# Optimization experiments

Hardware: AMD Instinct MI355X
Metric: run time of the kernel (lower is better)

## Reference

```python
import jax, jax.numpy as jnp
from jax import lax
import numpy as np

H, W = 240, 304
IN_CH, OUT_CH, K = 16, 32, 3
B = 8
N_PER = 65536
N = B * N_PER
CIN = IN_CH + 2  # pos + neg + features


def setup_inputs() -> dict:
    key = jax.random.key(0)
    k1, k2, k3, k4, k5 = jax.random.split(key, 5)
    # events columns: x, y, t in [0,1); polarity in {0,1}
    xyt = jax.random.uniform(k1, (N, 3), dtype=jnp.float32)
    pol = jax.random.randint(k2, (N, 1), 0, 2).astype(jnp.float32)
    events = jnp.concatenate([xyt, pol], axis=1)
    features = jax.random.normal(k3, (N, IN_CH), dtype=jnp.float32)
    offsets = (jnp.arange(1, B + 1, dtype=jnp.int64) * N_PER)  # cumulative counts
    # SubmanifoldConvolution params: one [CIN, OUT_CH] matrix per filter offset -> HWIO
    fan_in = K * K * CIN
    weight = jax.random.normal(k4, (K, K, CIN, OUT_CH), dtype=jnp.float32) / np.sqrt(fan_in)
    bias = jax.random.normal(k5, (OUT_CH,), dtype=jnp.float32) * 0.01
    return {"events": events, "features": features, "weight": weight,
            "bias": bias, "offsets": offsets}


def reference(events, features, weight, bias, offsets):
    n = events.shape[0]
    b = offsets.shape[0]
    # offset2batch: row i belongs to first sample whose cumulative offset exceeds i
    batch = jnp.searchsorted(offsets, jnp.arange(n, dtype=offsets.dtype), side="right").astype(jnp.int32)
    pos = events[:, 3:4]
    neg = 1.0 - pos
    sparse = jnp.concatenate([pos, neg, features], axis=1)  # [N, CIN]
    # yx = events[:, [1, 0]] scaled by (h, w), rounded to grid coords
    yi = jnp.clip(jnp.round(events[:, 1] * H).astype(jnp.int32), 0, H - 1)
    xi = jnp.clip(jnp.round(events[:, 0] * W).astype(jnp.int32), 0, W - 1)
    key = (batch * H + yi) * W + xi  # linear site id, [N]
    nseg = b * H * W
    # scn InputLayer mode=4: average features of duplicate coordinates
    feat_sum = jax.ops.segment_sum(sparse, key, num_segments=nseg)  # [nseg, CIN]
    cnt = jax.ops.segment_sum(jnp.ones((n,), sparse.dtype), key, num_segments=nseg)
    dense = feat_sum / jnp.maximum(cnt, 1.0)[:, None]
    dense = dense.reshape(b, H, W, CIN)  # zeros at inactive sites
    # Submanifold 3x3 conv: inactive neighbors are zero, so a dense SAME conv
    # evaluated only at active sites matches the submanifold rulebook math.
    out = lax.conv_general_dilated(dense, weight, window_strides=(1, 1),
                                   padding="SAME",
                                   dimension_numbers=("NHWC", "HWIO", "NHWC"))
    out = out.reshape(nseg, OUT_CH)
    # OutputLayer: read back per input row (active sites only), add bias there
    f = out[key] + bias  # [N, OUT_CH]
    return f
```

## Files before the change

### kernel.cpp

```cpp
#include <hip/hip_runtime.h>

#define Hh 240
#define Ww 304
#define IN_CH 16
#define OUT_CH 32
#define Bb 8
#define N_PER 65536
#define N_EV (Bb * N_PER)
#define CIN (IN_CH + 2)
#define NSEG (Bb * Hh * Ww)
#define NBLK 570

#define TW 32
#define TH 8
#define HW_ 34
#define HH_ 10
#define NXT_TILES 10
#define NYT_TILES 30
#define OPITCH 33

typedef __attribute__((ext_vector_type(8))) short bf16x8;
typedef __attribute__((ext_vector_type(4))) float f32x4;

__device__ __forceinline__ unsigned short f2bf(float x) {
  unsigned u = __float_as_uint(x);
  unsigned r = u + 0x7fffu + ((u >> 16) & 1u);
  return (unsigned short)(r >> 16);
}
__device__ __forceinline__ float bf2f(unsigned short b) {
  return __uint_as_float(((unsigned)b) << 16);
}

__global__ __launch_bounds__(256) void hist_rank_kernel(
    const float* __restrict__ events, const int* __restrict__ offsets,
    int* __restrict__ hist, int* __restrict__ keyArr, int* __restrict__ rankArr) {
  int i = blockIdx.x * blockDim.x + threadIdx.x;
  float4 ev = ((const float4*)events)[i];
  int yi = (int)rintf(ev.y * (float)Hh);
  yi = min(max(yi, 0), Hh - 1);
  int xi = (int)rintf(ev.x * (float)Ww);
  xi = min(max(xi, 0), Ww - 1);
  int b = 0;
#pragma unroll
  for (int j = 0; j < Bb; j++) b += (offsets[j] <= i) ? 1 : 0;
  int key = (b * Hh + yi) * Ww + xi;
  int pol = (ev.w != 0.0f) ? 1 : 0;
  keyArr[i] = key | (pol << 31);
  rankArr[i] = atomicAdd(&hist[key], 1);
}

__global__ __launch_bounds__(256) void scan1_kernel(
    const int* __restrict__ hist, int* __restrict__ baseLocal,
    int* __restrict__ blockSum) {
  __shared__ int lds[256];
  int b = blockIdx.x, t = threadIdx.x;
  int idx = b * 1024 + t * 4;
  int4 v = *(const int4*)(hist + idx);
  int s0 = v.x, s1 = s0 + v.y, s2 = s1 + v.z, s3 = s2 + v.w;
  lds[t] = s3;
  __syncthreads();
  int val = s3;
  for (int off = 1; off < 256; off <<= 1) {
    int n = (t >= off) ? lds[t - off] : 0;
    __syncthreads();
    val += n;
    lds[t] = val;
    __syncthreads();
  }
  int excl = val - s3;
  int4 o;
  o.x = excl; o.y = excl + s0; o.z = excl + s1; o.w = excl + s2;
  *(int4*)(baseLocal + idx) = o;
  if (t == 255) blockSum[b] = val;
}

__global__ __launch_bounds__(1024) void scan2_kernel(
    const int* __restrict__ blockSum, int* __restrict__ blockOffset) {
  __shared__ int lds[1024];
  int t = threadIdx.x;
  int v = (t < NBLK) ? blockSum[t] : 0;
  lds[t] = v;
  __syncthreads();
  int val = v;
  for (int off = 1; off < 1024; off <<= 1) {
    int n = (t >= off) ? lds[t - off] : 0;
    __syncthreads();
    val += n;
    lds[t] = val;
    __syncthreads();
  }
  if (t < NBLK) blockOffset[t] = val - v;
  if (t == 0) blockOffset[NBLK] = lds[1023];
}

__global__ __launch_bounds__(256) void prep_weights_kernel(
    const float* __restrict__ weight, unsigned short* __restrict__ wprep) {
  int tid = threadIdx.x;
#pragma unroll
  for (int it = 0; it < 24; it++) {
    int idx = it * 256 + tid;
    int ky = idx >> 11;
    int rem = idx & 2047;
    int n = rem >> 6;
    int kl = rem & 63;
    unsigned short v = 0;
    if (kl < 54) {
      int kx = kl / 18, ci = kl - kx * 18;
      v = f2bf(weight[((ky * 3 + kx) * CIN + ci) * OUT_CH + n]);
    }
    wprep[idx] = v;
  }
}

__global__ __launch_bounds__(256) void scatter_idx_kernel(
    const int* __restrict__ keyArr, const int* __restrict__ rankArr,
    const int* __restrict__ baseLocal, const int* __restrict__ blockOffset,
    int* __restrict__ sortedMeta) {
  int i = blockIdx.x * blockDim.x + threadIdx.x;
  int meta = keyArr[i];
  int key = meta & 0x7fffffff;
  int pos = baseLocal[key] + blockOffset[key >> 10] + rankArr[i];
  sortedMeta[pos] = i | (meta & 0x80000000);
}

__global__ __launch_bounds__(256) void fused_conv_kernel(
    const float* __restrict__ features, const int* __restrict__ sortedMeta,
    const int* __restrict__ baseLocal, const int* __restrict__ blockOffset,
    const unsigned short* __restrict__ wprep, const float* __restrict__ bias,
    float* __restrict__ out) {
  __shared__ unsigned smem[128 * OPITCH];
  __shared__ int ibase[TH * TW];
  __shared__ int icnt[TH * TW];

  int blk = blockIdx.x;
  int xt = blk % NXT_TILES;
  int rem = blk / NXT_TILES;
  int yt = rem % NYT_TILES;
  int b = rem / NYT_TILES;
  int x0 = xt * TW, y0 = yt * TH;
  int tid = threadIdx.x;

  if (tid < 12) smem[3060 + tid] = 0;

  for (int h = tid; h < HH_ * HW_; h += 256) {
    int hy = h / HW_, hx = h % HW_;
    int gy = y0 - 1 + hy, gx = x0 - 1 + hx;
    float acc[CIN];
#pragma unroll
    for (int k = 0; k < CIN; k++) acc[k] = 0.0f;
    int c = 0, base = 0;
    if (gy >= 0 && gy < Hh && gx >= 0 && gx < Ww) {
      int p = (b * Hh + gy) * Ww + gx;
      int bo = blockOffset[p >> 10];
      base = baseLocal[p] + bo;
      int nxt = ((p & 1023) != 1023) ? (baseLocal[p + 1] + bo)
                                     : blockOffset[(p >> 10) + 1];
      c = nxt - base;
      for (int j = 0; j < c; j++) {
        int e = sortedMeta[base + j];
        float pol = (float)((unsigned)e >> 31);
        acc[0] += pol;
        acc[1] += 1.0f - pol;
        const float4* f =
            (const float4*)(features + (size_t)(e & 0x7fffffff) * IN_CH);
        float4 f0 = f[0], f1 = f[1], f2 = f[2], f3 = f[3];
        acc[2] += f0.x;  acc[3] += f0.y;  acc[4] += f0.z;  acc[5] += f0.w;
        acc[6] += f1.x;  acc[7] += f1.y;  acc[8] += f1.z;  acc[9] += f1.w;
        acc[10] += f2.x; acc[11] += f2.y; acc[12] += f2.z; acc[13] += f2.w;
        acc[14] += f3.x; acc[15] += f3.y; acc[16] += f3.z; acc[17] += f3.w;
      }
    }
    float inv = 1.0f / fmaxf((float)c, 1.0f);
    unsigned* row = smem + 9 * h;
#pragma unroll
    for (int k = 0; k < 9; k++)
      row[k] = (unsigned)f2bf(acc[2 * k] * inv) |
               ((unsigned)f2bf(acc[2 * k + 1] * inv) << 16);
    if (hx >= 1 && hx <= TW && hy >= 1 && hy <= TH) {
      int t = (hy - 1) * TW + (hx - 1);
      ibase[t] = base;
      icnt[t] = c;
    }
  }
  __syncthreads();

  int wv = tid >> 6, lane = tid & 63;
  int quad = lane >> 4, lrow = lane & 15;

  f32x4 accf[4][2];
#pragma unroll
  for (int i = 0; i < 4; i++)
#pragma unroll
    for (int nt = 0; nt < 2; nt++) accf[i][nt] = (f32x4){0.f, 0.f, 0.f, 0.f};

  const unsigned* hp = smem;
#pragma unroll
  for (int ky = 0; ky < 3; ky++) {
    bf16x8 bfr[2][2];
#pragma unroll
    for (int kh = 0; kh < 2; kh++)
#pragma unroll
      for (int nt = 0; nt < 2; nt++) {
        int n = nt * 16 + lrow;
        bfr[kh][nt] = *(const bf16x8*)(wprep + ((ky * 32 + n) << 6) +
                                       kh * 32 + quad * 8);
      }
#pragma unroll
    for (int i = 0; i < 4; i++) {
      int t0 = (wv * 4 + i) * 16;
      int ox = (t0 & 31) + lrow;
      int oy = t0 >> 5;
      int idx0 = ((oy + ky) * HW_ + ox) * CIN;
#pragma unroll
      for (int kh = 0; kh < 2; kh++) {
        union { bf16x8 v; unsigned u[4]; } a;
        int ui = (idx0 >> 1) + kh * 16 + quad * 4;
        a.u[0] = hp[ui]; a.u[1] = hp[ui + 1];
        a.u[2] = hp[ui + 2]; a.u[3] = hp[ui + 3];
        accf[i][0] = __builtin_amdgcn_mfma_f32_16x16x32_bf16(
            a.v, bfr[kh][0], accf[i][0], 0, 0, 0);
        accf[i][1] = __builtin_amdgcn_mfma_f32_16x16x32_bf16(
            a.v, bfr[kh][1], accf[i][1], 0, 0, 0);
      }
    }
  }
  __syncthreads();

  float* outsh = (float*)smem;
  float bn0 = bias[lrow], bn1 = bias[16 + lrow];
  int gx = x0 + (tid & 31);
  int c = icnt[tid];
  int base = ibase[tid];
#pragma unroll
  for (int ch = 0; ch < 2; ch++) {
#pragma unroll
    for (int ii = 0; ii < 2; ii++) {
      int i = ch * 2 + ii;
      int lidx = ii * 16 + quad * 4;
      int row = wv * 32 + lidx;
#pragma unroll
      for (int r = 0; r < 4; r++) {
        outsh[(row + r) * OPITCH + lrow] = accf[i][0][r] + bn0;
        outsh[(row + r) * OPITCH + 16 + lrow] = accf[i][1][r] + bn1;
      }
    }
    __syncthreads();
    if (((tid >> 5) & 1) == ch && gx < Ww && c > 0) {
      int row = (tid >> 6) * 32 + ((tid & 63) - ch * 32);
      const float* rp = outsh + row * OPITCH;
      float4 o0 = make_float4(rp[0], rp[1], rp[2], rp[3]);
      float4 o1 = make_float4(rp[4], rp[5], rp[6], rp[7]);
      float4 o2 = make_float4(rp[8], rp[9], rp[10], rp[11]);
      float4 o3 = make_float4(rp[12], rp[13], rp[14], rp[15]);
      float4 o4 = make_float4(rp[16], rp[17], rp[18], rp[19]);
      float4 o5 = make_float4(rp[20], rp[21], rp[22], rp[23]);
      float4 o6 = make_float4(rp[24], rp[25], rp[26], rp[27]);
      float4 o7 = make_float4(rp[28], rp[29], rp[30], rp[31]);
      for (int j = 0; j < c; j++) {
        int ev = sortedMeta[base + j] & 0x7fffffff;
        float4* op = (float4*)(out + (size_t)ev * OUT_CH);
        op[0] = o0; op[1] = o1; op[2] = o2; op[3] = o3;
        op[4] = o4; op[5] = o5; op[6] = o6; op[7] = o7;
      }
    }
    __syncthreads();
  }
}

extern "C" void kernel_launch(void* const* d_in, const int* in_sizes, int n_in,
                              void* d_out, int out_size, void* d_ws,
                              size_t ws_size, hipStream_t stream) {
  const float* events = (const float*)d_in[0];
  const float* features = (const float*)d_in[1];
  const float* weight = (const float*)d_in[2];
  const float* bias = (const float*)d_in[3];
  const int* offsets = (const int*)d_in[4];
  float* out = (float*)d_out;

  int* sortedMeta = (int*)d_ws;
  int* keyArr = sortedMeta + N_EV;
  int* rankArr = keyArr + N_EV;
  int* hist = rankArr + N_EV;
  int* baseLocal = hist + NSEG;
  int* blockOffset = baseLocal + NSEG;
  int* blockSum = blockOffset + 1024;
  unsigned short* wprep = (unsigned short*)(blockSum + 1024);

  hipMemsetAsync(hist, 0, (size_t)NSEG * sizeof(int), stream);

  hist_rank_kernel<<<N_EV / 256, 256, 0, stream>>>(events, offsets, hist,
                                                   keyArr, rankArr);
  prep_weights_kernel<<<1, 256, 0, stream>>>(weight, wprep);
  scan1_kernel<<<NBLK, 256, 0, stream>>>(hist, baseLocal, blockSum);
  scan2_kernel<<<1, 1024, 0, stream>>>(blockSum, blockOffset);
  scatter_idx_kernel<<<N_EV / 256, 256, 0, stream>>>(
      keyArr, rankArr, baseLocal, blockOffset, sortedMeta);
  fused_conv_kernel<<<Bb * NYT_TILES * NXT_TILES, 256, 0, stream>>>(
      features, sortedMeta, baseLocal, blockOffset, wprep, bias, out);
}
```

Baseline: 193.2 us.

## Distribute halo event gathering across threads with LDS atomics; fuse weight prep into scan2

The conv kernel's halo gather no longer gives each thread one pixel to loop over serially. It now builds per-row prefix sums of event counts and hands out individual events to threads. Each thread binary-searches for its event's pixel and accumulates features into a shared-memory fp32 buffer with LDS atomics. This evens out load across threads and makes feature reads more coalesced, at the cost of atomic contention, extra syncs and more LDS use, which may lower occupancy. Weight preparation is also merged into the scan2 launch as a second block, removing one kernel launch.

```diff
diff --git a/kernel.cpp b/kernel.cpp
--- a/kernel.cpp
+++ b/kernel.cpp
@@ -15,6 +15,7 @@
 #define TH 8
 #define HW_ 34
 #define HH_ 10
+#define HALO_PIX (HH_ * HW_)
 #define NXT_TILES 10
 #define NYT_TILES 30
 #define OPITCH 33
@@ -26,9 +27,6 @@
   unsigned u = __float_as_uint(x);
   unsigned r = u + 0x7fffu + ((u >> 16) & 1u);
   return (unsigned short)(r >> 16);
-}
-__device__ __forceinline__ float bf2f(unsigned short b) {
-  return __uint_as_float(((unsigned)b) << 16);
 }
 
 __global__ __launch_bounds__(256) void hist_rank_kernel(
@@ -74,10 +72,28 @@
   if (t == 255) blockSum[b] = val;
 }
 
-__global__ __launch_bounds__(1024) void scan2_kernel(
-    const int* __restrict__ blockSum, int* __restrict__ blockOffset) {
+__global__ __launch_bounds__(1024) void scan2_weights_kernel(
+    const int* __restrict__ blockSum, int* __restrict__ blockOffset,
+    const float* __restrict__ weight, unsigned short* __restrict__ wprep) {
+  int t = threadIdx.x;
+  if (blockIdx.x == 1) {
+#pragma unroll
+    for (int it = 0; it < 6; it++) {
+      int idx = it * 1024 + t;
+      int ky = idx >> 11;
+      int rem = idx & 2047;
+      int n = rem >> 6;
+      int kl = rem & 63;
+      unsigned short v = 0;
+      if (kl < 54) {
+        int kx = kl / 18, ci = kl - kx * 18;
+        v = f2bf(weight[((ky * 3 + kx) * CIN + ci) * OUT_CH + n]);
+      }
+      wprep[idx] = v;
+    }
+    return;
+  }
   __shared__ int lds[1024];
-  int t = threadIdx.x;
   int v = (t < NBLK) ? blockSum[t] : 0;
   lds[t] = v;
   __syncthreads();
@@ -91,25 +107,6 @@
   }
   if (t < NBLK) blockOffset[t] = val - v;
   if (t == 0) blockOffset[NBLK] = lds[1023];
-}
-
-__global__ __launch_bounds__(256) void prep_weights_kernel(
-    const float* __restrict__ weight, unsigned short* __restrict__ wprep) {
-  int tid = threadIdx.x;
-#pragma unroll
-  for (int it = 0; it < 24; it++) {
-    int idx = it * 256 + tid;
-    int ky = idx >> 11;
-    int rem = idx & 2047;
-    int n = rem >> 6;
-    int kl = rem & 63;
-    unsigned short v = 0;
-    if (kl < 54) {
-      int kx = kl / 18, ci = kl - kx * 18;
-      v = f2bf(weight[((ky * 3 + kx) * CIN + ci) * OUT_CH + n]);
-    }
-    wprep[idx] = v;
-  }
 }
 
 __global__ __launch_bounds__(256) void scatter_idx_kernel(
@@ -128,9 +125,12 @@
     const int* __restrict__ baseLocal, const int* __restrict__ blockOffset,
     const unsigned short* __restrict__ wprep, const float* __restrict__ bias,
     float* __restrict__ out) {
-  __shared__ unsigned smem[128 * OPITCH];
-  __shared__ int ibase[TH * TW];
-  __shared__ int icnt[TH * TW];
+  __shared__ float haloAcc[HALO_PIX * CIN];
+  __shared__ unsigned haloBf[3072];
+  __shared__ int pixBase[HALO_PIX];
+  __shared__ int pixCnt[HALO_PIX];
+  __shared__ int rowStart[HH_];
+  __shared__ int rowPfx[HH_ + 1];
 
   int blk = blockIdx.x;
   int xt = blk % NXT_TILES;
@@ -140,47 +140,79 @@
   int x0 = xt * TW, y0 = yt * TH;
   int tid = threadIdx.x;
 
-  if (tid < 12) smem[3060 + tid] = 0;
-
-  for (int h = tid; h < HH_ * HW_; h += 256) {
+  if (tid < 12) haloBf[3060 + tid] = 0;
+
+  for (int h = tid; h < HALO_PIX; h += 256) {
     int hy = h / HW_, hx = h % HW_;
     int gy = y0 - 1 + hy, gx = x0 - 1 + hx;
-    float acc[CIN];
-#pragma unroll
-    for (int k = 0; k < CIN; k++) acc[k] = 0.0f;
-    int c = 0, base = 0;
-    if (gy >= 0 && gy < Hh && gx >= 0 && gx < Ww) {
+    int base = 0, c = 0;
+    bool valid = (gy >= 0 && gy < Hh && gx >= 0 && gx < Ww);
+    if (valid) {
       int p = (b * Hh + gy) * Ww + gx;
       int bo = blockOffset[p >> 10];
       base = baseLocal[p] + bo;
       int nxt = ((p & 1023) != 1023) ? (baseLocal[p + 1] + bo)
                                      : blockOffset[(p >> 10) + 1];
       c = nxt - base;
-      for (int j = 0; j < c; j++) {
-        int e = sortedMeta[base + j];
-        float pol = (float)((unsigned)e >> 31);
-        acc[0] += pol;
-        acc[1] += 1.0f - pol;
-        const float4* f =
-            (const float4*)(features + (size_t)(e & 0x7fffffff) * IN_CH);
-        float4 f0 = f[0], f1 = f[1], f2 = f[2], f3 = f[3];
-        acc[2] += f0.x;  acc[3] += f0.y;  acc[4] += f0.z;  acc[5] += f0.w;
-        acc[6] += f1.x;  acc[7] += f1.y;  acc[8] += f1.z;  acc[9] += f1.w;
-        acc[10] += f2.x; acc[11] += f2.y; acc[12] += f2.z; acc[13] += f2.w;
-        acc[14] += f3.x; acc[15] += f3.y; acc[16] += f3.z; acc[17] += f3.w;
-      }
-    }
-    float inv = 1.0f / fmaxf((float)c, 1.0f);
-    unsigned* row = smem + 9 * h;
+    }
+    pixBase[h] = valid ? base : (gx < 0 ? 0 : 0x7fffffff);
+    pixCnt[h] = c;
+#pragma unroll
+    for (int k = 0; k < CIN; k++) haloAcc[h * CIN + k] = 0.0f;
+  }
+  __syncthreads();
+
+  if (tid < HH_) {
+    int s = 0;
+#pragma unroll
+    for (int x = 0; x < HW_; x++) s += pixCnt[tid * HW_ + x];
+    rowPfx[tid + 1] = s;
+    rowStart[tid] = pixBase[tid * HW_ + ((x0 == 0) ? 1 : 0)];
+  }
+  if (tid == 0) rowPfx[0] = 0;
+  __syncthreads();
+  if (tid == 0) {
+#pragma unroll
+    for (int r = 1; r <= HH_; r++) rowPfx[r] += rowPfx[r - 1];
+  }
+  __syncthreads();
+  int T = rowPfx[HH_];
+
+  for (int t = tid; t < T; t += 256) {
+    int r = 0;
+    while (r < HH_ - 1 && rowPfx[r + 1] <= t) ++r;
+    int q = rowStart[r] + (t - rowPfx[r]);
+    int lo = r * HW_, hi = lo + HW_ - 1;
+    while (lo < hi) {
+      int mid = (lo + hi + 1) >> 1;
+      if (pixBase[mid] <= q) lo = mid; else hi = mid - 1;
+    }
+    int meta = sortedMeta[q];
+    float pol = (float)((unsigned)meta >> 31);
+    int e = meta & 0x7fffffff;
+    const float4* f = (const float4*)(features + (size_t)e * IN_CH);
+    float4 f0 = f[0], f1 = f[1], f2 = f[2], f3 = f[3];
+    float* hA = haloAcc + lo * CIN;
+    atomicAdd(hA + 0, pol);
+    atomicAdd(hA + 1, 1.0f - pol);
+    atomicAdd(hA + 2, f0.x);  atomicAdd(hA + 3, f0.y);
+    atomicAdd(hA + 4, f0.z);  atomicAdd(hA + 5, f0.w);
+    atomicAdd(hA + 6, f1.x);  atomicAdd(hA + 7, f1.y);
+    atomicAdd(hA + 8, f1.z);  atomicAdd(hA + 9, f1.w);
+    atomicAdd(hA + 10, f2.x); atomicAdd(hA + 11, f2.y);
+    atomicAdd(hA + 12, f2.z); atomicAdd(hA + 13, f2.w);
+    atomicAdd(hA + 14, f3.x); atomicAdd(hA + 15, f3.y);
+    atomicAdd(hA + 16, f3.z); atomicAdd(hA + 17, f3.w);
+  }
+  __syncthreads();
+
+  for (int h = tid; h < HALO_PIX; h += 256) {
+    float inv = 1.0f / fmaxf((float)pixCnt[h], 1.0f);
+    unsigned* row = haloBf + 9 * h;
 #pragma unroll
     for (int k = 0; k < 9; k++)
-      row[k] = (unsigned)f2bf(acc[2 * k] * inv) |
-               ((unsigned)f2bf(acc[2 * k + 1] * inv) << 16);
-    if (hx >= 1 && hx <= TW && hy >= 1 && hy <= TH) {
-      int t = (hy - 1) * TW + (hx - 1);
-      ibase[t] = base;
-      icnt[t] = c;
-    }
+      row[k] = (unsigned)f2bf(haloAcc[h * CIN + 2 * k] * inv) |
+               ((unsigned)f2bf(haloAcc[h * CIN + 2 * k + 1] * inv) << 16);
   }
   __syncthreads();
 
@@ -193,7 +225,7 @@
 #pragma unroll
     for (int nt = 0; nt < 2; nt++) accf[i][nt] = (f32x4){0.f, 0.f, 0.f, 0.f};
 
-  const unsigned* hp = smem;
+  const unsigned* hp = haloBf;
 #pragma unroll
   for (int ky = 0; ky < 3; ky++) {
     bf16x8 bfr[2][2];
@@ -226,11 +258,12 @@
   }
   __syncthreads();
 
-  float* outsh = (float*)smem;
+  float* outsh = haloAcc;
   float bn0 = bias[lrow], bn1 = bias[16 + lrow];
   int gx = x0 + (tid & 31);
-  int c = icnt[tid];
-  int base = ibase[tid];
+  int hint = ((tid >> 5) + 1) * HW_ + (tid & 31) + 1;
+  int c = pixCnt[hint];
+  int base = pixBase[hint];
 #pragma unroll
   for (int ch = 0; ch < 2; ch++) {
 #pragma unroll
@@ -290,9 +323,9 @@
 
   hist_rank_kernel<<<N_EV / 256, 256, 0, stream>>>(events, offsets, hist,
                                                    keyArr, rankArr);
-  prep_weights_kernel<<<1, 256, 0, stream>>>(weight, wprep);
   scan1_kernel<<<NBLK, 256, 0, stream>>>(hist, baseLocal, blockSum);
-  scan2_kernel<<<1, 1024, 0, stream>>>(blockSum, blockOffset);
+  scan2_weights_kernel<<<2, 1024, 0, stream>>>(blockSum, blockOffset, weight,
+                                               wprep);
   scatter_idx_kernel<<<N_EV / 256, 256, 0, stream>>>(
       keyArr, rankArr, baseLocal, blockOffset, sortedMeta);
   fused_conv_kernel<<<Bb * NYT_TILES * NXT_TILES, 256, 0, stream>>>(
```

New measurement: 239.5 us. 1.24x slower.

## Scatter bf16 feature records in sorted order and fuse weight prep into scan

Applied to the files above, without the earlier changes.

The scatter kernel now writes each event's polarity/index metadata and bf16-packed features into a record array ordered by grid site, so the conv's halo accumulation reads contiguous records instead of gathering fp32 features by random index. Key and rank are stored together as an int2, weight preparation runs as a second block of the scan2 launch, and the halo loop issues both pixel lookups before accumulating. This trades random gathers in the conv for heavier random writes in scatter and rounds features to bf16 before averaging, which adds precision error.

```diff
diff --git a/kernel.cpp b/kernel.cpp
--- a/kernel.cpp
+++ b/kernel.cpp
@@ -15,6 +15,7 @@
 #define TH 8
 #define HW_ 34
 #define HH_ 10
+#define HALO_PIX (HH_ * HW_)
 #define NXT_TILES 10
 #define NYT_TILES 30
 #define OPITCH 33
@@ -30,10 +31,13 @@
 __device__ __forceinline__ float bf2f(unsigned short b) {
   return __uint_as_float(((unsigned)b) << 16);
 }
+__device__ __forceinline__ unsigned pk2(float a, float b) {
+  return (unsigned)f2bf(a) | ((unsigned)f2bf(b) << 16);
+}
 
 __global__ __launch_bounds__(256) void hist_rank_kernel(
     const float* __restrict__ events, const int* __restrict__ offsets,
-    int* __restrict__ hist, int* __restrict__ keyArr, int* __restrict__ rankArr) {
+    int* __restrict__ hist, int2* __restrict__ kr) {
   int i = blockIdx.x * blockDim.x + threadIdx.x;
   float4 ev = ((const float4*)events)[i];
   int yi = (int)rintf(ev.y * (float)Hh);
@@ -45,8 +49,8 @@
   for (int j = 0; j < Bb; j++) b += (offsets[j] <= i) ? 1 : 0;
   int key = (b * Hh + yi) * Ww + xi;
   int pol = (ev.w != 0.0f) ? 1 : 0;
-  keyArr[i] = key | (pol << 31);
-  rankArr[i] = atomicAdd(&hist[key], 1);
+  int rank = atomicAdd(&hist[key], 1);
+  kr[i] = make_int2(key | (pol << 31), rank);
 }
 
 __global__ __launch_bounds__(256) void scan1_kernel(
@@ -74,10 +78,28 @@
   if (t == 255) blockSum[b] = val;
 }
 
-__global__ __launch_bounds__(1024) void scan2_kernel(
-    const int* __restrict__ blockSum, int* __restrict__ blockOffset) {
+__global__ __launch_bounds__(1024) void scan2_weights_kernel(
+    const int* __restrict__ blockSum, int* __restrict__ blockOffset,
+    const float* __restrict__ weight, unsigned short* __restrict__ wprep) {
+  int t = threadIdx.x;
+  if (blockIdx.x == 1) {
+#pragma unroll
+    for (int it = 0; it < 6; it++) {
+      int idx = it * 1024 + t;
+      int ky = idx >> 11;
+      int rem = idx & 2047;
+      int n = rem >> 6;
+      int kl = rem & 63;
+      unsigned short v = 0;
+      if (kl < 54) {
+        int kx = kl / 18, ci = kl - kx * 18;
+        v = f2bf(weight[((ky * 3 + kx) * CIN + ci) * OUT_CH + n]);
+      }
+      wprep[idx] = v;
+    }
+    return;
+  }
   __shared__ int lds[1024];
-  int t = threadIdx.x;
   int v = (t < NBLK) ? blockSum[t] : 0;
   lds[t] = v;
   __syncthreads();
@@ -93,38 +115,55 @@
   if (t == 0) blockOffset[NBLK] = lds[1023];
 }
 
-__global__ __launch_bounds__(256) void prep_weights_kernel(
-    const float* __restrict__ weight, unsigned short* __restrict__ wprep) {
-  int tid = threadIdx.x;
-#pragma unroll
-  for (int it = 0; it < 24; it++) {
-    int idx = it * 256 + tid;
-    int ky = idx >> 11;
-    int rem = idx & 2047;
-    int n = rem >> 6;
-    int kl = rem & 63;
-    unsigned short v = 0;
-    if (kl < 54) {
-      int kx = kl / 18, ci = kl - kx * 18;
-      v = f2bf(weight[((ky * 3 + kx) * CIN + ci) * OUT_CH + n]);
-    }
-    wprep[idx] = v;
-  }
-}
-
-__global__ __launch_bounds__(256) void scatter_idx_kernel(
-    const int* __restrict__ keyArr, const int* __restrict__ rankArr,
+__global__ __launch_bounds__(256) void scatter_rec_kernel(
+    const float* __restrict__ features, const int2* __restrict__ kr,
     const int* __restrict__ baseLocal, const int* __restrict__ blockOffset,
-    int* __restrict__ sortedMeta) {
+    uint4* __restrict__ sortedRec, int* __restrict__ sortedMeta) {
   int i = blockIdx.x * blockDim.x + threadIdx.x;
-  int meta = keyArr[i];
-  int key = meta & 0x7fffffff;
-  int pos = baseLocal[key] + blockOffset[key >> 10] + rankArr[i];
-  sortedMeta[pos] = i | (meta & 0x80000000);
+  int2 m = kr[i];
+  int key = m.x & 0x7fffffff;
+  int pos = baseLocal[key] + blockOffset[key >> 10] + m.y;
+  const float4* f = (const float4*)(features + (size_t)i * IN_CH);
+  float4 f0 = f[0], f1 = f[1], f2 = f[2], f3 = f[3];
+  unsigned meta = (unsigned)i | ((unsigned)m.x & 0x80000000u);
+  uint4* R = sortedRec + (size_t)pos * 3;
+  R[0] = make_uint4(meta, pk2(f0.x, f0.y), pk2(f0.z, f0.w), pk2(f1.x, f1.y));
+  R[1] = make_uint4(pk2(f1.z, f1.w), pk2(f2.x, f2.y), pk2(f2.z, f2.w),
+                    pk2(f3.x, f3.y));
+  R[2] = make_uint4(pk2(f3.z, f3.w), 0, 0, 0);
+  sortedMeta[pos] = (int)meta;
+}
+
+__device__ __forceinline__ void accum_pixel(unsigned* smem,
+                                            const uint4* __restrict__ sortedRec,
+                                            int h, int base, int c) {
+  float acc[CIN];
+#pragma unroll
+  for (int k = 0; k < CIN; k++) acc[k] = 0.0f;
+  for (int j = 0; j < c; j++) {
+    const uint4* R = sortedRec + (size_t)(base + j) * 3;
+    uint4 r0 = R[0], r1 = R[1];
+    unsigned d8 = ((const unsigned*)R)[8];
+    float pol = (float)(r0.x >> 31);
+    acc[0] += pol;
+    acc[1] += 1.0f - pol;
+    acc[2]  += bf2f((unsigned short)r0.y);  acc[3]  += bf2f((unsigned short)(r0.y >> 16));
+    acc[4]  += bf2f((unsigned short)r0.z);  acc[5]  += bf2f((unsigned short)(r0.z >> 16));
+    acc[6]  += bf2f((unsigned short)r0.w);  acc[7]  += bf2f((unsigned short)(r0.w >> 16));
+    acc[8]  += bf2f((unsigned short)r1.x);  acc[9]  += bf2f((unsigned short)(r1.x >> 16));
+    acc[10] += bf2f((unsigned short)r1.y);  acc[11] += bf2f((unsigned short)(r1.y >> 16));
+    acc[12] += bf2f((unsigned short)r1.z);  acc[13] += bf2f((unsigned short)(r1.z >> 16));
+    acc[14] += bf2f((unsigned short)r1.w);  acc[15] += bf2f((unsigned short)(r1.w >> 16));
+    acc[16] += bf2f((unsigned short)d8);    acc[17] += bf2f((unsigned short)(d8 >> 16));
+  }
+  float inv = 1.0f / fmaxf((float)c, 1.0f);
+  unsigned* row = smem + 9 * h;
+#pragma unroll
+  for (int k = 0; k < 9; k++) row[k] = pk2(acc[2 * k] * inv, acc[2 * k + 1] * inv);
 }
 
 __global__ __launch_bounds__(256) void fused_conv_kernel(
-    const float* __restrict__ features, const int* __restrict__ sortedMeta,
+    const uint4* __restrict__ sortedRec, const int* __restrict__ sortedMeta,
     const int* __restrict__ baseLocal, const int* __restrict__ blockOffset,
     const unsigned short* __restrict__ wprep, const float* __restrict__ bias,
     float* __restrict__ out) {
@@ -142,44 +181,49 @@
 
   if (tid < 12) smem[3060 + tid] = 0;
 
-  for (int h = tid; h < HH_ * HW_; h += 256) {
-    int hy = h / HW_, hx = h % HW_;
+  int hA = tid, hB = tid + 256;
+  bool hasB = hB < HALO_PIX;
+  int baseA = 0, cA = 0, baseB = 0, cB = 0;
+  {
+    int hy = hA / HW_, hx = hA % HW_;
     int gy = y0 - 1 + hy, gx = x0 - 1 + hx;
-    float acc[CIN];
-#pragma unroll
-    for (int k = 0; k < CIN; k++) acc[k] = 0.0f;
-    int c = 0, base = 0;
     if (gy >= 0 && gy < Hh && gx >= 0 && gx < Ww) {
       int p = (b * Hh + gy) * Ww + gx;
       int bo = blockOffset[p >> 10];
-      base = baseLocal[p] + bo;
+      baseA = baseLocal[p] + bo;
       int nxt = ((p & 1023) != 1023) ? (baseLocal[p + 1] + bo)
                                      : blockOffset[(p >> 10) + 1];
-      c = nxt - base;
-      for (int j = 0; j < c; j++) {
-        int e = sortedMeta[base + j];
-        float pol = (float)((unsigned)e >> 31);
-        acc[0] += pol;
-        acc[1] += 1.0f - pol;
-        const float4* f =
-            (const float4*)(features + (size_t)(e & 0x7fffffff) * IN_CH);
-        float4 f0 = f[0], f1 = f[1], f2 = f[2], f3 = f[3];
-        acc[2] += f0.x;  acc[3] += f0.y;  acc[4] += f0.z;  acc[5] += f0.w;
-        acc[6] += f1.x;  acc[7] += f1.y;  acc[8] += f1.z;  acc[9] += f1.w;
-        acc[10] += f2.x; acc[11] += f2.y; acc[12] += f2.z; acc[13] += f2.w;
-        acc[14] += f3.x; acc[15] += f3.y; acc[16] += f3.z; acc[17] += f3.w;
-      }
-    }
-    float inv = 1.0f / fmaxf((float)c, 1.0f);
-    unsigned* row = smem + 9 * h;
-#pragma unroll
-    for (int k = 0; k < 9; k++)
-      row[k] = (unsigned)f2bf(acc[2 * k] * inv) |
-               ((unsigned)f2bf(acc[2 * k + 1] * inv) << 16);
+      cA = nxt - baseA;
+    }
+  }
+  if (hasB) {
+    int hy = hB / HW_, hx = hB % HW_;
+    int gy = y0 - 1 + hy, gx = x0 - 1 + hx;
+    if (gy >= 0 && gy < Hh && gx >= 0 && gx < Ww) {
+      int p = (b * Hh + gy) * Ww + gx;
+      int bo = blockOffset[p >> 10];
+      baseB = baseLocal[p] + bo;
+      int nxt = ((p & 1023) != 1023) ? (baseLocal[p + 1] + bo)
+                                     : blockOffset[(p >> 10) + 1];
+      cB = nxt - baseB;
+    }
+  }
+  accum_pixel(smem, sortedRec, hA, baseA, cA);
+  if (hasB) accum_pixel(smem, sortedRec, hB, baseB, cB);
+  {
+    int hy = hA / HW_, hx = hA % HW_;
     if (hx >= 1 && hx <= TW && hy >= 1 && hy <= TH) {
       int t = (hy - 1) * TW + (hx - 1);
-      ibase[t] = base;
-      icnt[t] = c;
+      ibase[t] = baseA;
+      icnt[t] = cA;
+    }
+  }
+  if (hasB) {
+    int hy = hB / HW_, hx = hB % HW_;
+    if (hx >= 1 && hx <= TW && hy >= 1 && hy <= TH) {
+      int t = (hy - 1) * TW + (hx - 1);
+      ibase[t] = baseB;
+      icnt[t] = cB;
     }
   }
   __syncthreads();
@@ -277,10 +321,10 @@
   const int* offsets = (const int*)d_in[4];
   float* out = (float*)d_out;
 
-  int* sortedMeta = (int*)d_ws;
-  int* keyArr = sortedMeta + N_EV;
-  int* rankArr = keyArr + N_EV;
-  int* hist = rankArr + N_EV;
+  uint4* sortedRec = (uint4*)d_ws;
+  int* sortedMeta = (int*)(sortedRec + (size_t)N_EV * 3);
+  int2* kr = (int2*)(sortedMeta + N_EV);
+  int* hist = (int*)(kr + N_EV);
   int* baseLocal = hist + NSEG;
   int* blockOffset = baseLocal + NSEG;
   int* blockSum = blockOffset + 1024;
@@ -288,13 +332,12 @@
 
   hipMemsetAsync(hist, 0, (size_t)NSEG * sizeof(int), stream);
 
-  hist_rank_kernel<<<N_EV / 256, 256, 0, stream>>>(events, offsets, hist,
-                                                   keyArr, rankArr);
-  prep_weights_kernel<<<1, 256, 0, stream>>>(weight, wprep);
+  hist_rank_kernel<<<N_EV / 256, 256, 0, stream>>>(events, offsets, hist, kr);
   scan1_kernel<<<NBLK, 256, 0, stream>>>(hist, baseLocal, blockSum);
-  scan2_kernel<<<1, 1024, 0, stream>>>(blockSum, blockOffset);
-  scatter_idx_kernel<<<N_EV / 256, 256, 0, stream>>>(
-      keyArr, rankArr, baseLocal, blockOffset, sortedMeta);
+  scan2_weights_kernel<<<2, 1024, 0, stream>>>(blockSum, blockOffset, weight,
+                                               wprep);
+  scatter_rec_kernel<<<N_EV / 256, 256, 0, stream>>>(
+      features, kr, baseLocal, blockOffset, sortedRec, sortedMeta);
   fused_conv_kernel<<<Bb * NYT_TILES * NXT_TILES, 256, 0, stream>>>(
-      features, sortedMeta, baseLocal, blockOffset, wprep, bias, out);
-}
+      sortedRec, sortedMeta, baseLocal, blockOffset, wprep, bias, out);
+}
```

Result: no change. 194.9 us (+0.9%).
